# Kernel optimization log

Hardware: AMD Instinct MI355X
Metric: run time of the kernel (lower is better)

## Reference

```python
import jax, jax.numpy as jnp
import numpy as np

D_SCALE_INT = 100
MOTION_TH = 0.25 * D_SCALE_INT  # 25.0
EPS = 1e-05


def _forward_warp(im0, flow):
    B, C, H, W = im0.shape
    N = B * H * W
    dtype = im0.dtype

    gx = jnp.arange(W, dtype=dtype)[None, None, :]   # [1,1,W]
    gy = jnp.arange(H, dtype=dtype)[None, :, None]   # [1,H,1]
    x_dest = gx + flow[..., 0]                        # [B,H,W]
    y_dest = gy + flow[..., 1]                        # [B,H,W]

    mag_sq = flow[..., 0] ** 2 + flow[..., 1] ** 2
    d = (D_SCALE_INT * jnp.sqrt(mag_sq)).astype(jnp.int32)  # [B,H,W]

    x_f = jnp.floor(x_dest).astype(jnp.int32)
    y_f = jnp.floor(y_dest).astype(jnp.int32)
    x_c = x_f + 1
    y_c = y_f + 1

    xf_f = x_f.astype(dtype); yf_f = y_f.astype(dtype)
    xc_f = x_c.astype(dtype); yc_f = y_c.astype(dtype)
    nw_k = (xc_f - x_dest) * (yc_f - y_dest)
    ne_k = (x_dest - xf_f) * (yc_f - y_dest)
    sw_k = (xc_f - x_dest) * (y_dest - yf_f)
    se_k = (x_dest - xf_f) * (y_dest - yf_f)

    valid = (x_f >= 0) & (x_c <= W) & (y_f >= 0) & (y_c <= H)  # [B,H,W]

    x_fc = jnp.clip(x_f, 0, W - 1); y_fc = jnp.clip(y_f, 0, H - 1)
    x_cc = jnp.clip(x_c, 0, W - 1); y_cc = jnp.clip(y_c, 0, H - 1)

    b_base = (jnp.arange(B, dtype=jnp.int32) * (H * W))[:, None, None]  # [B,1,1]
    corners = [
        (nw_k, y_fc, x_fc),
        (ne_k, y_fc, x_cc),
        (sw_k, y_cc, x_fc),
        (se_k, y_cc, x_cc),
    ]
    sp_idx = [b_base + yy * W + xx for (_, yy, xx) in corners]  # each [B,H,W]

    # scatter-max depth test (buffer init 0, d >= 0, so masked-out -> 0 is a no-op)
    d_buf = jnp.zeros((N,), dtype=jnp.int32)
    for (k, _, _), idx in zip(corners, sp_idx):
        cond = (k >= 0.25) & valid
        d_buf = d_buf.at[idx.reshape(-1)].max(
            jnp.where(cond, d, jnp.int32(0)).reshape(-1))

    d_buf_f = d_buf.astype(dtype)
    d_f = d.astype(dtype)

    # gather depth, pass-test, scatter-add bilinear splat
    im1_buf = jnp.zeros((C, N), dtype=dtype)
    wght_buf = jnp.zeros((N,), dtype=dtype)
    im0_cn = jnp.transpose(im0, (1, 0, 2, 3)).reshape(C, N)  # [C, B*H*W]
    for (k, _, _), idx in zip(corners, sp_idx):
        flat_idx = idx.reshape(-1)
        d_gather = d_buf_f[flat_idx].reshape(d.shape)  # [B,H,W]
        cond = (k >= 0.25) & (d_gather - d_f <= MOTION_TH) & valid
        w = (k * cond.astype(dtype)).reshape(-1)       # [N]
        im1_buf = im1_buf.at[:, flat_idx].add(im0_cn * w[None, :])
        wght_buf = wght_buf.at[flat_idx].add(w)

    im1_buffer = jnp.transpose(im1_buf.reshape(C, B, H, W), (1, 0, 2, 3))
    wght = (wght_buf / C).reshape(B, 1, H, W)
    im1 = im1_buffer / jnp.maximum(wght, EPS)
    return im1


def setup_inputs() -> dict:
    key = jax.random.key(0)
    k1, k2 = jax.random.split(key)
    B, C, H, W = 4, 3, 1080, 1920
    im0 = jax.random.normal(k1, (B, C, H, W), dtype=jnp.float32)
    # scale flow to realistic pixel displacements (~20 px)
    flow = jax.random.normal(k2, (B, H, W, 2), dtype=jnp.float32) * 20.0
    return {"im0": im0, "flow": flow}


def reference(im0, flow):
    return _forward_warp(im0, flow)
```

## Files before the change

### kernel.cpp

```cpp
#include <hip/hip_runtime.h>

constexpr int B = 4, C = 3, H = 1080, W = 1920;
constexpr int HW = H * W;
constexpr int N = B * HW;
constexpr float MOTION_TH = 25.0f;
constexpr float EPS = 1e-5f;

constexpr float W_SCALE = 1024.0f;
constexpr float V_SCALE = 256.0f;

constexpr int   TILE_W = 160, TILE_H = 36;
constexpr int   MARG   = 48;
constexpr float NEAR_TH = 47.0f;
constexpr int   REG_W  = TILE_W + 2 * MARG;
constexpr int   REG_H  = TILE_H + 2 * MARG;
constexpr int   CELLS  = TILE_W * TILE_H;
constexpr int   TX = W / TILE_W;
constexpr int   TY = H / TILE_H;
constexpr int   NTILES = B * TX * TY;
constexpr int   WL_CAP = 9216;

struct Splat {
    bool  valid;
    int   di;
    float df;
    float k[4];
    int   cx[4], cy[4];
};

__device__ __forceinline__ Splat make_splat(int x, int y, float fx, float fy) {
    Splat s;
    float xd = (float)x + fx;
    float yd = (float)y + fy;
    float xf = floorf(xd), yf = floorf(yd);
    int xfi = (int)xf, yfi = (int)yf;
    int xci = xfi + 1, yci = yfi + 1;
    s.valid = (xfi >= 0) & (xci <= W) & (yfi >= 0) & (yci <= H);
    s.di = (int)(100.0f * sqrtf(fx * fx + fy * fy));
    s.df = (float)s.di;
    float wx1 = xd - xf, wx0 = (xf + 1.0f) - xd;
    float wy1 = yd - yf, wy0 = (yf + 1.0f) - yd;
    int x0 = min(max(xfi, 0), W - 1), x1 = min(max(xci, 0), W - 1);
    int y0 = min(max(yfi, 0), H - 1), y1 = min(max(yci, 0), H - 1);
    s.k[0] = wx0 * wy0; s.cx[0] = x0; s.cy[0] = y0;
    s.k[1] = wx1 * wy0; s.cx[1] = x1; s.cy[1] = y0;
    s.k[2] = wx0 * wy1; s.cx[2] = x0; s.cy[2] = y1;
    s.k[3] = wx1 * wy1; s.cx[3] = x1; s.cy[3] = y1;
    return s;
}

__device__ __forceinline__ bool is_near(float fx, float fy) {
    return (fabsf(fx) <= NEAR_TH) && (fabsf(fy) <= NEAR_TH);
}

__global__ void far_depth(const float* __restrict__ flow, int* __restrict__ dbuf) {
    int n = blockIdx.x * blockDim.x + threadIdx.x;
    if (n >= N) return;
    float2 f = reinterpret_cast<const float2*>(flow)[n];
    if (is_near(f.x, f.y)) return;
    int b   = n / HW;
    int pix = n - b * HW;
    int y   = pix / W;
    int x   = pix - y * W;
    Splat s = make_splat(x, y, f.x, f.y);
    if (!s.valid) return;
    int base = b * HW;
    #pragma unroll
    for (int c = 0; c < 4; ++c)
        if (s.k[c] >= 0.25f)
            atomicMax(&dbuf[base + s.cy[c] * W + s.cx[c]], s.di);
}

__global__ __launch_bounds__(1024, 8) void tile_fused(
        const float* __restrict__ im0,
        const float* __restrict__ flow,
        int* __restrict__ dbuf,
        unsigned long long* __restrict__ acc) {
    __shared__ unsigned long long aloc[CELLS];
    __shared__ unsigned short     du16[CELLS];
    __shared__ unsigned short     wl[WL_CAP];
    __shared__ int                wl_cnt;
    int* dstage = (int*)aloc;

    const int t = threadIdx.x;
    int tile = (blockIdx.x & 7) * (NTILES / 8) + (blockIdx.x >> 3);
    int txi  = tile % TX;
    int tmp  = tile / TX;
    int tyi  = tmp % TY;
    int b    = tmp / TY;
    const int x0t = txi * TILE_W, y0t = tyi * TILE_H;
    const int base = b * HW;
    const float2* flow2 = reinterpret_cast<const float2*>(flow);

    if (t == 0) wl_cnt = 0;
    for (int i = t; i < CELLS; i += 1024) dstage[i] = 0;
    __syncthreads();

    const int   rxc   = t & (REG_W - 1);
    const int   gx    = x0t - MARG + rxc;
    const bool  colok = (gx >= 0) & (gx < W);
    const int   gy_hi = min(H, y0t + TILE_H + MARG);
    int gys = y0t - MARG + (t >> 8);
    if (gys < 0) gys += (-gys + 3) & ~3;
    const float gxf  = (float)gx;
    const float bxlo = (float)(x0t - 1),    bxhi = (float)(x0t + TILE_W);
    const float bylo = (float)(y0t - 1),    byhi = (float)(y0t + TILE_H);
    const int   lane = t & 63;

    if (colok) {
        const float2* fp = flow2 + base + (long)gys * W + gx;
        float2 fnext = (gys < gy_hi) ? *fp : float2{0.0f, 0.0f};
        for (int gy = gys; gy < gy_hi; gy += 4, fp += 4 * W) {
            float2 f = fnext;
            if (gy + 4 < gy_hi) fnext = fp[4 * W];
            float xd = gxf + f.x;
            float yd = (float)gy + f.y;
            bool hit = (xd >= bxlo) & (xd < bxhi) & (yd >= bylo) & (yd < byhi)
                     & (fabsf(f.x) <= NEAR_TH) & (fabsf(f.y) <= NEAR_TH);
            unsigned long long m = __ballot(hit);
            if (hit) {
                int rank = __popcll(m & ((1ull << lane) - 1ull));
                int bslot = 0;
                if (rank == 0) bslot = atomicAdd(&wl_cnt, __popcll(m));
                bslot = __shfl(bslot, __ffsll((long long)m) - 1);
                int slot = bslot + rank;
                if (slot < WL_CAP)
                    wl[slot] = (unsigned short)(((gy - (y0t - MARG)) << 8) | rxc);
            }
        }
    }
    __syncthreads();
    const int cnt = min(wl_cnt, WL_CAP);

    for (int w = t; w < cnt; w += 1024) {
        int e  = wl[w];
        int rx = e & 255, ry = e >> 8;
        int gx2 = x0t - MARG + rx, gy2 = y0t - MARG + ry;
        float2 f = flow2[base + gy2 * W + gx2];
        float xd = (float)gx2 + f.x, yd = (float)gy2 + f.y;
        float xf = floorf(xd), yf = floorf(yd);
        int xfi = (int)xf, yfi = (int)yf;
        int xci = xfi + 1, yci = yfi + 1;
        if (!((xfi >= 0) & (xci <= W) & (yfi >= 0) & (yci <= H))) continue;
        float wx1 = xd - xf, wx0 = (xf + 1.0f) - xd;
        float wy1 = yd - yf, wy0 = (yf + 1.0f) - yd;
        int X0 = min(max(xfi, 0), W - 1), X1 = min(max(xci, 0), W - 1);
        int Y0 = min(max(yfi, 0), H - 1), Y1 = min(max(yci, 0), H - 1);
        int lx0 = X0 - x0t, lx1 = X1 - x0t, ly0 = Y0 - y0t, ly1 = Y1 - y0t;
        bool ox0 = (unsigned)lx0 < (unsigned)TILE_W;
        bool ox1 = (unsigned)lx1 < (unsigned)TILE_W;
        bool oy0 = (unsigned)ly0 < (unsigned)TILE_H;
        bool oy1 = (unsigned)ly1 < (unsigned)TILE_H;
        float k0 = wx0 * wy0, k1 = wx1 * wy0, k2 = wx0 * wy1, k3 = wx1 * wy1;
        bool m0 = (k0 >= 0.25f) & ox0 & oy0;
        bool m1 = (k1 >= 0.25f) & ox1 & oy0;
        bool m2 = (k2 >= 0.25f) & ox0 & oy1;
        bool m3 = (k3 >= 0.25f) & ox1 & oy1;
        if (!(m0 | m1 | m2 | m3)) continue;
        int di = (int)(100.0f * sqrtf(f.x * f.x + f.y * f.y));
        if (m0) atomicMax(&dstage[ly0 * TILE_W + lx0], di);
        if (m1) atomicMax(&dstage[ly0 * TILE_W + lx1], di);
        if (m2) atomicMax(&dstage[ly1 * TILE_W + lx0], di);
        if (m3) atomicMax(&dstage[ly1 * TILE_W + lx1], di);
    }
    __syncthreads();

    for (int i = t; i < CELLS; i += 1024) {
        int ly = i / TILE_W, lx = i - ly * TILE_W;
        int g  = base + (y0t + ly) * W + (x0t + lx);
        int dm = max(dstage[i], dbuf[g]);
        dbuf[g] = dm;
        du16[i] = (unsigned short)min(dm, 65535);
    }
    __syncthreads();

    for (int i = t; i < CELLS; i += 1024) aloc[i] = 0ull;
    __syncthreads();

    for (int w = t; w < cnt; w += 1024) {
        int e  = wl[w];
        int rx = e & 255, ry = e >> 8;
        int gx2 = x0t - MARG + rx, gy2 = y0t - MARG + ry;
        int pix = gy2 * W + gx2;
        float2 f = flow2[base + pix];
        float xd = (float)gx2 + f.x, yd = (float)gy2 + f.y;
        float xf = floorf(xd), yf = floorf(yd);
        int xfi = (int)xf, yfi = (int)yf;
        int xci = xfi + 1, yci = yfi + 1;
        if (!((xfi >= 0) & (xci <= W) & (yfi >= 0) & (yci <= H))) continue;
        float wx1 = xd - xf, wx0 = (xf + 1.0f) - xd;
        float wy1 = yd - yf, wy0 = (yf + 1.0f) - yd;
        int X0 = min(max(xfi, 0), W - 1), X1 = min(max(xci, 0), W - 1);
        int Y0 = min(max(yfi, 0), H - 1), Y1 = min(max(yci, 0), H - 1);
        int lx0 = X0 - x0t, lx1 = X1 - x0t, ly0 = Y0 - y0t, ly1 = Y1 - y0t;
        bool ox0 = (unsigned)lx0 < (unsigned)TILE_W;
        bool ox1 = (unsigned)lx1 < (unsigned)TILE_W;
        bool oy0 = (unsigned)ly0 < (unsigned)TILE_H;
        bool oy1 = (unsigned)ly1 < (unsigned)TILE_H;
        float k0 = wx0 * wy0, k1 = wx1 * wy0, k2 = wx0 * wy1, k3 = wx1 * wy1;
        bool m0 = (k0 >= 0.25f) & ox0 & oy0;
        bool m1 = (k1 >= 0.25f) & ox1 & oy0;
        bool m2 = (k2 >= 0.25f) & ox0 & oy1;
        bool m3 = (k3 >= 0.25f) & ox1 & oy1;
        if (!(m0 | m1 | m2 | m3)) continue;
        int di = (int)(100.0f * sqrtf(f.x * f.x + f.y * f.y));
        float df = (float)di;
        int l00 = ly0 * TILE_W + lx0, l01 = ly0 * TILE_W + lx1;
        int l10 = ly1 * TILE_W + lx0, l11 = ly1 * TILE_W + lx1;
        bool g0 = m0 && ((float)du16[l00] - df <= MOTION_TH);
        bool g1 = m1 && ((float)du16[l01] - df <= MOTION_TH);
        bool g2 = m2 && ((float)du16[l10] - df <= MOTION_TH);
        bool g3 = m3 && ((float)du16[l11] - df <= MOTION_TH);
        if (!(g0 | g1 | g2 | g3)) continue;
        float v0 = im0[(b * C + 0) * HW + pix];
        float v1 = im0[(b * C + 1) * HW + pix];
        float v2 = im0[(b * C + 2) * HW + pix];
        float kk[4] = { k0, k1, k2, k3 };
        int   ll[4] = { l00, l01, l10, l11 };
        bool  gg[4] = { g0, g1, g2, g3 };
        #pragma unroll
        for (int c = 0; c < 4; ++c) {
            if (!gg[c]) continue;
            float k = kk[c];
            long long wq = (long long)__float2int_rn(k * W_SCALE);
            long long rq = (long long)__float2int_rn(v0 * k * V_SCALE);
            long long gq = (long long)__float2int_rn(v1 * k * V_SCALE);
            long long bq = (long long)__float2int_rn(v2 * k * V_SCALE);
            unsigned long long S =
                (unsigned long long)(wq + (rq << 16) + (gq << 32) + (bq << 48));
            atomicAdd(&aloc[ll[c]], S);
        }
    }
    __syncthreads();

    for (int i = t; i < CELLS; i += 1024) {
        int ly = i / TILE_W, lx = i - ly * TILE_W;
        acc[base + (y0t + ly) * W + (x0t + lx)] = aloc[i];
    }
}

__global__ void far_splat(const float* __restrict__ im0,
                          const float* __restrict__ flow,
                          const int* __restrict__ dbuf,
                          unsigned long long* __restrict__ acc) {
    int n = blockIdx.x * blockDim.x + threadIdx.x;
    if (n >= N) return;
    float2 f = reinterpret_cast<const float2*>(flow)[n];
    if (is_near(f.x, f.y)) return;
    int b   = n / HW;
    int pix = n - b * HW;
    int y   = pix / W;
    int x   = pix - y * W;
    Splat s = make_splat(x, y, f.x, f.y);
    if (!s.valid) return;
    float v0 = im0[(b * C + 0) * HW + pix];
    float v1 = im0[(b * C + 1) * HW + pix];
    float v2 = im0[(b * C + 2) * HW + pix];
    int base = b * HW;
    #pragma unroll
    for (int c = 0; c < 4; ++c) {
        if (s.k[c] < 0.25f) continue;
        int idx = base + s.cy[c] * W + s.cx[c];
        float dg = (float)dbuf[idx];
        if (dg - s.df <= MOTION_TH) {
            float k = s.k[c];
            long long wq = (long long)__float2int_rn(k * W_SCALE);
            long long rq = (long long)__float2int_rn(v0 * k * V_SCALE);
            long long gq = (long long)__float2int_rn(v1 * k * V_SCALE);
            long long bq = (long long)__float2int_rn(v2 * k * V_SCALE);
            long long S  = wq + (rq << 16) + (gq << 32) + (bq << 48);
            atomicAdd(&acc[idx], (unsigned long long)S);
        }
    }
}

__global__ void norm_pass(const unsigned long long* __restrict__ acc,
                          float* __restrict__ out) {
    int n = blockIdx.x * blockDim.x + threadIdx.x;
    if (n >= N) return;
    int b   = n / HW;
    int pix = n - b * HW;

    long long T = (long long)acc[n];
    int wq = (int)(T & 0xffff);
    long long T1 = (T - wq) >> 16;
    int rq = (int)(((T1 & 0xffff) ^ 0x8000) - 0x8000);
    long long T2 = (T1 - rq) >> 16;
    int gq = (int)(((T2 & 0xffff) ^ 0x8000) - 0x8000);
    long long T3 = (T2 - gq) >> 16;
    int bq = (int)T3;

    float w  = (float)wq * (1.0f / W_SCALE);
    float r  = (float)rq * (1.0f / V_SCALE);
    float g  = (float)gq * (1.0f / V_SCALE);
    float bl = (float)bq * (1.0f / V_SCALE);

    float den = fmaxf(w * (1.0f / 3.0f), EPS);
    float inv = 1.0f / den;
    float* p = out + (size_t)b * C * HW + pix;
    p[0]      = r  * inv;
    p[HW]     = g  * inv;
    p[2 * HW] = bl * inv;
}

extern "C" void kernel_launch(void* const* d_in, const int* in_sizes, int n_in,
                              void* d_out, int out_size, void* d_ws, size_t ws_size,
                              hipStream_t stream) {
    const float* im0  = (const float*)d_in[0];
    const float* flow = (const float*)d_in[1];
    float* out = (float*)d_out;

    unsigned long long* acc = (unsigned long long*)d_ws;
    int* dbuf = (int*)((char*)d_ws + (size_t)N * 8);

    (void)hipMemsetAsync(dbuf, 0, (size_t)N * 4, stream);

    const int block = 256;
    const int grid  = (N + block - 1) / block;

    far_depth <<<grid,   block, 0, stream>>>(flow, dbuf);
    tile_fused<<<NTILES, 1024,  0, stream>>>(im0, flow, dbuf, acc);
    far_splat <<<grid,   block, 0, stream>>>(im0, flow, dbuf, acc);
    norm_pass <<<grid,   block, 0, stream>>>(acc, out);
}
```

Measured before the change: 397.5 us.

## Retune tile geometry and vectorize far-pass and normalization kernels

Changes the tile to 128x45 with a 64-pixel margin and raises the near threshold to 63, so more pixels are handled in the shared-memory tile kernel and fewer go through the global-atomic far path. The far_depth and far_splat kernels become grid-stride loops over float4 flow loads that process two pixels per iteration with a fixed grid. norm_pass reads two accumulators at once and writes float2 stores. The larger margin grows the halo region per tile and the shared worklist capacity shrinks, which may hurt occupancy or overflow the worklist when many pixels are near.

```diff
diff --git a/kernel.cpp b/kernel.cpp
--- a/kernel.cpp
+++ b/kernel.cpp
@@ -9,16 +9,15 @@
 constexpr float W_SCALE = 1024.0f;
 constexpr float V_SCALE = 256.0f;
 
-constexpr int   TILE_W = 160, TILE_H = 36;
-constexpr int   MARG   = 48;
-constexpr float NEAR_TH = 47.0f;
+constexpr int   TILE_W = 128, TILE_H = 45;
+constexpr int   MARG   = 64;
+constexpr float NEAR_TH = 63.0f;
 constexpr int   REG_W  = TILE_W + 2 * MARG;
-constexpr int   REG_H  = TILE_H + 2 * MARG;
 constexpr int   CELLS  = TILE_W * TILE_H;
 constexpr int   TX = W / TILE_W;
 constexpr int   TY = H / TILE_H;
 constexpr int   NTILES = B * TX * TY;
-constexpr int   WL_CAP = 9216;
+constexpr int   WL_CAP = 8192;
 
 struct Splat {
     bool  valid;
@@ -54,21 +53,29 @@
 }
 
 __global__ void far_depth(const float* __restrict__ flow, int* __restrict__ dbuf) {
-    int n = blockIdx.x * blockDim.x + threadIdx.x;
-    if (n >= N) return;
-    float2 f = reinterpret_cast<const float2*>(flow)[n];
-    if (is_near(f.x, f.y)) return;
-    int b   = n / HW;
-    int pix = n - b * HW;
-    int y   = pix / W;
-    int x   = pix - y * W;
-    Splat s = make_splat(x, y, f.x, f.y);
-    if (!s.valid) return;
-    int base = b * HW;
-    #pragma unroll
-    for (int c = 0; c < 4; ++c)
-        if (s.k[c] >= 0.25f)
-            atomicMax(&dbuf[base + s.cy[c] * W + s.cx[c]], s.di);
+    const float4* flow4 = reinterpret_cast<const float4*>(flow);
+    int stride = gridDim.x * blockDim.x;
+    for (int i = blockIdx.x * blockDim.x + threadIdx.x; i < N / 2; i += stride) {
+        float4 q = flow4[i];
+        #pragma unroll
+        for (int h = 0; h < 2; ++h) {
+            float fx = h ? q.z : q.x;
+            float fy = h ? q.w : q.y;
+            if (is_near(fx, fy)) continue;
+            int n   = 2 * i + h;
+            int b   = n / HW;
+            int pix = n - b * HW;
+            int y   = pix / W;
+            int x   = pix - y * W;
+            Splat s = make_splat(x, y, fx, fy);
+            if (!s.valid) continue;
+            int base = b * HW;
+            #pragma unroll
+            for (int c = 0; c < 4; ++c)
+                if (s.k[c] >= 0.25f)
+                    atomicMax(&dbuf[base + s.cy[c] * W + s.cx[c]], s.di);
+        }
+    }
 }
 
 __global__ __launch_bounds__(1024, 8) void tile_fused(
@@ -243,64 +250,77 @@
                           const float* __restrict__ flow,
                           const int* __restrict__ dbuf,
                           unsigned long long* __restrict__ acc) {
-    int n = blockIdx.x * blockDim.x + threadIdx.x;
-    if (n >= N) return;
-    float2 f = reinterpret_cast<const float2*>(flow)[n];
-    if (is_near(f.x, f.y)) return;
+    const float4* flow4 = reinterpret_cast<const float4*>(flow);
+    int stride = gridDim.x * blockDim.x;
+    for (int i = blockIdx.x * blockDim.x + threadIdx.x; i < N / 2; i += stride) {
+        float4 q = flow4[i];
+        #pragma unroll
+        for (int h = 0; h < 2; ++h) {
+            float fx = h ? q.z : q.x;
+            float fy = h ? q.w : q.y;
+            if (is_near(fx, fy)) continue;
+            int n   = 2 * i + h;
+            int b   = n / HW;
+            int pix = n - b * HW;
+            int y   = pix / W;
+            int x   = pix - y * W;
+            Splat s = make_splat(x, y, fx, fy);
+            if (!s.valid) continue;
+            float v0 = im0[(b * C + 0) * HW + pix];
+            float v1 = im0[(b * C + 1) * HW + pix];
+            float v2 = im0[(b * C + 2) * HW + pix];
+            int base = b * HW;
+            #pragma unroll
+            for (int c = 0; c < 4; ++c) {
+                if (s.k[c] < 0.25f) continue;
+                int idx = base + s.cy[c] * W + s.cx[c];
+                float dg = (float)dbuf[idx];
+                if (dg - s.df <= MOTION_TH) {
+                    float k = s.k[c];
+                    long long wq = (long long)__float2int_rn(k * W_SCALE);
+                    long long rq = (long long)__float2int_rn(v0 * k * V_SCALE);
+                    long long gq = (long long)__float2int_rn(v1 * k * V_SCALE);
+                    long long bq = (long long)__float2int_rn(v2 * k * V_SCALE);
+                    long long S  = wq + (rq << 16) + (gq << 32) + (bq << 48);
+                    atomicAdd(&acc[idx], (unsigned long long)S);
+                }
+            }
+        }
+    }
+}
+
+__global__ void norm_pass(const unsigned long long* __restrict__ acc,
+                          float* __restrict__ out) {
+    int i = blockIdx.x * blockDim.x + threadIdx.x;
+    if (i >= N / 2) return;
+    ulonglong2 T2 = reinterpret_cast<const ulonglong2*>(acc)[i];
+    int n   = 2 * i;
     int b   = n / HW;
     int pix = n - b * HW;
-    int y   = pix / W;
-    int x   = pix - y * W;
-    Splat s = make_splat(x, y, f.x, f.y);
-    if (!s.valid) return;
-    float v0 = im0[(b * C + 0) * HW + pix];
-    float v1 = im0[(b * C + 1) * HW + pix];
-    float v2 = im0[(b * C + 2) * HW + pix];
-    int base = b * HW;
+
+    float res[6];
     #pragma unroll
-    for (int c = 0; c < 4; ++c) {
-        if (s.k[c] < 0.25f) continue;
-        int idx = base + s.cy[c] * W + s.cx[c];
-        float dg = (float)dbuf[idx];
-        if (dg - s.df <= MOTION_TH) {
-            float k = s.k[c];
-            long long wq = (long long)__float2int_rn(k * W_SCALE);
-            long long rq = (long long)__float2int_rn(v0 * k * V_SCALE);
-            long long gq = (long long)__float2int_rn(v1 * k * V_SCALE);
-            long long bq = (long long)__float2int_rn(v2 * k * V_SCALE);
-            long long S  = wq + (rq << 16) + (gq << 32) + (bq << 48);
-            atomicAdd(&acc[idx], (unsigned long long)S);
-        }
-    }
-}
-
-__global__ void norm_pass(const unsigned long long* __restrict__ acc,
-                          float* __restrict__ out) {
-    int n = blockIdx.x * blockDim.x + threadIdx.x;
-    if (n >= N) return;
-    int b   = n / HW;
-    int pix = n - b * HW;
-
-    long long T = (long long)acc[n];
-    int wq = (int)(T & 0xffff);
-    long long T1 = (T - wq) >> 16;
-    int rq = (int)(((T1 & 0xffff) ^ 0x8000) - 0x8000);
-    long long T2 = (T1 - rq) >> 16;
-    int gq = (int)(((T2 & 0xffff) ^ 0x8000) - 0x8000);
-    long long T3 = (T2 - gq) >> 16;
-    int bq = (int)T3;
-
-    float w  = (float)wq * (1.0f / W_SCALE);
-    float r  = (float)rq * (1.0f / V_SCALE);
-    float g  = (float)gq * (1.0f / V_SCALE);
-    float bl = (float)bq * (1.0f / V_SCALE);
-
-    float den = fmaxf(w * (1.0f / 3.0f), EPS);
-    float inv = 1.0f / den;
+    for (int h = 0; h < 2; ++h) {
+        long long T = (long long)(h ? T2.y : T2.x);
+        int wq = (int)(T & 0xffff);
+        long long T1 = (T - wq) >> 16;
+        int rq = (int)(((T1 & 0xffff) ^ 0x8000) - 0x8000);
+        long long Tt = (T1 - rq) >> 16;
+        int gq = (int)(((Tt & 0xffff) ^ 0x8000) - 0x8000);
+        long long T3 = (Tt - gq) >> 16;
+        int bq = (int)T3;
+
+        float w  = (float)wq * (1.0f / W_SCALE);
+        float den = fmaxf(w * (1.0f / 3.0f), EPS);
+        float inv = 1.0f / den;
+        res[0 + h] = (float)rq * (1.0f / V_SCALE) * inv;
+        res[2 + h] = (float)gq * (1.0f / V_SCALE) * inv;
+        res[4 + h] = (float)bq * (1.0f / V_SCALE) * inv;
+    }
     float* p = out + (size_t)b * C * HW + pix;
-    p[0]      = r  * inv;
-    p[HW]     = g  * inv;
-    p[2 * HW] = bl * inv;
+    *reinterpret_cast<float2*>(p)          = float2{res[0], res[1]};
+    *reinterpret_cast<float2*>(p + HW)     = float2{res[2], res[3]};
+    *reinterpret_cast<float2*>(p + 2 * HW) = float2{res[4], res[5]};
 }
 
 extern "C" void kernel_launch(void* const* d_in, const int* in_sizes, int n_in,
@@ -316,10 +336,10 @@
     (void)hipMemsetAsync(dbuf, 0, (size_t)N * 4, stream);
 
     const int block = 256;
-    const int grid  = (N + block - 1) / block;
-
-    far_depth <<<grid,   block, 0, stream>>>(flow, dbuf);
+    const int sgrid = 2048;
+
+    far_depth <<<sgrid,  block, 0, stream>>>(flow, dbuf);
     tile_fused<<<NTILES, 1024,  0, stream>>>(im0, flow, dbuf, acc);
-    far_splat <<<grid,   block, 0, stream>>>(im0, flow, dbuf, acc);
-    norm_pass <<<grid,   block, 0, stream>>>(acc, out);
-}
+    far_splat <<<sgrid,  block, 0, stream>>>(im0, flow, dbuf, acc);
+    norm_pass <<<(N / 2 + block - 1) / block, block, 0, stream>>>(acc, out);
+}
```

New measurement: 374.1 us. 5.9% less time.
